# Kernel optimization log

Measured on AMD Instinct MI355X. Metric: run time of the kernel, lower is better.

## Reference

```python
import jax, jax.numpy as jnp
import numpy as np

CUTOFF = 2.0
LOG2 = float(np.log(2.0))

def ssp(x):
    # shifted softplus: softplus(x) - log(2)
    return jax.nn.softplus(x) - LOG2

def setup_inputs() -> dict:
    key = jax.random.key(0)
    ks = jax.random.split(key, 12)
    N, E, H, F, G = 10000, 320000, 256, 256, 50
    x = jax.random.normal(ks[0], (N, H), dtype=jnp.float32)
    edge_index = jax.random.randint(ks[1], (2, E), 0, N, dtype=jnp.int64)
    edge_weight = jax.random.normal(ks[2], (E, 3), dtype=jnp.float32)
    edge_attr = jax.random.normal(ks[3], (E, G), dtype=jnp.float32)
    s = lambda fan_in: 1.0 / np.sqrt(fan_in)
    mlp_w1 = jax.random.uniform(ks[4], (G, F), jnp.float32, -s(G), s(G))
    mlp_b1 = jax.random.uniform(ks[5], (F,), jnp.float32, -s(G), s(G))
    mlp_w2 = jax.random.uniform(ks[6], (F, F), jnp.float32, -s(F), s(F))
    mlp_b2 = jax.random.uniform(ks[7], (F,), jnp.float32, -s(F), s(F))
    lin1_w = jax.random.uniform(ks[8], (H, F), jnp.float32, -s(H), s(H))
    lin2_w = jax.random.uniform(ks[9], (F, H), jnp.float32, -s(F), s(F))
    lin2_b = jax.random.uniform(ks[10], (H,), jnp.float32, -s(F), s(F))
    return {"x": x, "edge_index": edge_index, "edge_weight": edge_weight,
            "edge_attr": edge_attr, "mlp_w1": mlp_w1, "mlp_b1": mlp_b1,
            "mlp_w2": mlp_w2, "mlp_b2": mlp_b2, "lin1_w": lin1_w,
            "lin2_w": lin2_w, "lin2_b": lin2_b}

def reference(x, edge_index, edge_weight, edge_attr,
              mlp_w1, mlp_b1, mlp_w2, mlp_b2, lin1_w, lin2_w, lin2_b):
    N = x.shape[0]
    # cutoff envelope on edge distances
    distances = jnp.linalg.norm(edge_weight, axis=1)                 # [E]
    C = 0.5 * (jnp.cos(distances * jnp.pi / CUTOFF) + 1.0)
    C = C * (distances <= CUTOFF)                                    # [E]
    # edge filter MLP
    W = ssp(edge_attr @ mlp_w1 + mlp_b1) @ mlp_w2 + mlp_b2           # [E, F]
    W = W * C[:, None]
    i, j = edge_index[0], edge_index[1]
    messages = W * (x[j] @ lin1_w)                                   # [E, F]
    agg = jax.ops.segment_sum(messages, i, num_segments=N)           # [N, F]
    h = ssp(agg @ lin2_w + lin2_b)                                   # [N, H]
    return x + h
```

## Files before the change

### kernel.cpp

```cpp
#include <hip/hip_runtime.h>
#include <hip/hip_bf16.h>
#include <stdint.h>

#define HF 256
#define GG 50
#define LOG2E 1.44269504088896341f
#define LN2   0.69314718055994531f

typedef __attribute__((ext_vector_type(8))) short bf16x8;
typedef __attribute__((ext_vector_type(4))) short bf16x4;
typedef __attribute__((ext_vector_type(4))) float f32x4;

__device__ __forceinline__ uint32_t f2bf2u(float a, float b){
    __hip_bfloat162 h = __float22bfloat162_rn(make_float2(a, b));
    union { __hip_bfloat162 h; uint32_t u; } v; v.h = h; return v.u;
}
__device__ __forceinline__ float bf2f(short s){
    union { uint32_t u; float f; } v; v.u = ((uint32_t)(uint16_t)s) << 16;
    return v.f;
}

__device__ __forceinline__ void pack_natural(const float* __restrict__ B,
                                             short* __restrict__ Bp,
                                             int idx, int KT, int kmax, float scale)
{
    int lane = idx & 63;
    int kt   = (idx >> 6) & (KT - 1);
    int ntg  = idx >> (6 + (KT == 2 ? 1 : 3));
    int col  = ntg * 16 + (lane & 15);
    int k0   = kt * 32 + (lane >> 4) * 8;
    uint32_t u[4];
#pragma unroll
    for (int jj = 0; jj < 4; ++jj) {
        int ka = k0 + 2*jj, kb = ka + 1;
        float a = (ka < kmax) ? B[(size_t)ka * HF + col] * scale : 0.f;
        float b = (kb < kmax) ? B[(size_t)kb * HF + col] * scale : 0.f;
        u[jj] = f2bf2u(a, b);
    }
    *(uint4*)&Bp[(size_t)idx * 8] = *(uint4*)u;
}

__global__ __launch_bounds__(256)
void prep_kernel(const float* __restrict__ w1, const float* __restrict__ b1,
                 const float* __restrict__ w2, const float* __restrict__ b2,
                 const float* __restrict__ lin1, const float* __restrict__ lin2,
                 short* __restrict__ w1p, short* __restrict__ w2p,
                 short* __restrict__ lin1p, short* __restrict__ lin2p,
                 float* __restrict__ b2p,
                 const float* __restrict__ x, short* __restrict__ x_bf, int nx8,
                 const int* __restrict__ eidx, int* __restrict__ cnt, int E,
                 float* __restrict__ agg, int nAgg4, int gConv, int gHist)
{
    int b = blockIdx.x, tid = threadIdx.x;
    if (b < 8) {
        int idx  = b * 256 + tid;
        int lane = idx & 63;
        int kt   = (idx >> 6) & 1;
        int ntg  = idx >> 7;
        int col  = ntg * 16 + (lane & 15);
        int k0   = kt * 32 + (lane >> 4) * 8;
        uint32_t u[4];
#pragma unroll
        for (int jj = 0; jj < 4; ++jj) {
            int ka = k0 + 2*jj, kb = ka + 1;
            float va = (ka < GG) ? w1[(size_t)ka * HF + col] * LOG2E
                                 : ((ka == GG) ? b1[col] * LOG2E : 0.f);
            float vb = (kb < GG) ? w1[(size_t)kb * HF + col] * LOG2E
                                 : ((kb == GG) ? b1[col] * LOG2E : 0.f);
            u[jj] = f2bf2u(va, vb);
        }
        *(uint4*)&w1p[(size_t)idx * 8] = *(uint4*)u;
    } else if (b < 40) {
        int idx = (b - 8) * 256 + tid;
        int lane = idx & 63;
        int kt   = (idx >> 6) & 7;
        int ntg  = idx >> 9;
        int col  = ntg * 16 + (lane & 15);
        int s0   = kt * 32 + (lane >> 4) * 8;
        uint32_t u[4];
#pragma unroll
        for (int jj = 0; jj < 4; ++jj) {
            int sa = s0 + 2*jj, sb = sa + 1;
            int fa = (sa >> 5) * 32 + (sa & 1) * 16 + ((sa & 31) >> 1);
            int fb = (sb >> 5) * 32 + (sb & 1) * 16 + ((sb & 31) >> 1);
            u[jj] = f2bf2u(w2[(size_t)fa * HF + col] * LN2,
                           w2[(size_t)fb * HF + col] * LN2);
        }
        *(uint4*)&w2p[(size_t)idx * 8] = *(uint4*)u;
    } else if (b < 72) {
        pack_natural(lin1, lin1p, (b - 40) * 256 + tid, 8, HF, 1.0f);
    } else if (b < 104) {
        pack_natural(lin2, lin2p, (b - 72) * 256 + tid, 8, HF, LOG2E);
    } else if (b == 104) {
        int f = tid;
        float s = 0.f;
        for (int k = 0; k < HF; ++k) {
            uint32_t r = f2bf2u(w2[(size_t)k * HF + f] * LN2, 0.f);
            s += bf2f((short)(r & 0xFFFF));
        }
        b2p[f] = b2[f] - s;
    } else if (b < 105 + gConv) {
        int idx = (b - 105) * 256 + tid;
        if (idx < nx8) {
            const float* xp = x + (size_t)idx * 8;
            float4 p0 = *(const float4*)(xp);
            float4 p1 = *(const float4*)(xp + 4);
            uint32_t u[4] = { f2bf2u(p0.x, p0.y), f2bf2u(p0.z, p0.w),
                              f2bf2u(p1.x, p1.y), f2bf2u(p1.z, p1.w) };
            *(uint4*)&x_bf[(size_t)idx * 8] = *(uint4*)u;
        }
    } else if (b < 105 + gConv + gHist) {
        int e = (b - 105 - gConv) * 256 + tid;
        if (e < E) atomicAdd(&cnt[eidx[e]], 1);
    } else {
        int idx = (b - 105 - gConv - gHist) * 256 + tid;
        if (idx < nAgg4) ((float4*)agg)[idx] = make_float4(0.f, 0.f, 0.f, 0.f);
    }
}

__global__ __launch_bounds__(256)
void scan_gemm_kernel(const int* __restrict__ cnt, int* __restrict__ row,
                      int* __restrict__ cursor, int N, int E,
                      const short* __restrict__ x_bf, const short* __restrict__ lin1p,
                      short* __restrict__ y_p)
{
    const int tid = threadIdx.x;
    if (blockIdx.x == 0) {
        __shared__ int part[256];
        const int CH = (N + 255) / 256;
        int lo = tid * CH;
        int hi = min(lo + CH, N);
        int s = 0;
        for (int n = lo; n < hi; ++n) s += cnt[n];
        part[tid] = s;
        __syncthreads();
        for (int off = 1; off < 256; off <<= 1) {
            int v = (tid >= off) ? part[tid - off] : 0;
            __syncthreads();
            part[tid] += v;
            __syncthreads();
        }
        int acc = part[tid] - s;
        for (int n = lo; n < hi; ++n) {
            row[n] = acc; cursor[n] = acc;
            acc += cnt[n];
        }
        if (tid == 255) row[N] = E;
        return;
    }
    const int blk    = blockIdx.x - 1;
    const int rowblk = blk >> 1;
    const int fh     = blk & 1;
    const int lane = tid & 63;
    const int w    = tid >> 6;
    const int l15  = lane & 15;
    const int quad = lane >> 4;
    const int row0 = rowblk * 64;

    f32x4 acc[4][2];
#pragma unroll
    for (int mt = 0; mt < 4; ++mt)
#pragma unroll
        for (int nt = 0; nt < 2; ++nt) acc[mt][nt] = (f32x4){0.f,0.f,0.f,0.f};

#pragma unroll 2
    for (int kt = 0; kt < 8; ++kt) {
        bf16x8 af[4];
#pragma unroll
        for (int mt = 0; mt < 4; ++mt) {
            int r = row0 + mt * 16 + l15;
            int rl = (r < N) ? r : 0;
            af[mt] = *(const bf16x8*)&x_bf[(size_t)rl * HF + kt * 32 + quad * 8];
        }
#pragma unroll
        for (int nt = 0; nt < 2; ++nt) {
            int ntg = fh * 8 + w * 2 + nt;
            bf16x8 bfr = *(const bf16x8*)&lin1p[(size_t)((ntg*8+kt)*64+lane)*8];
#pragma unroll
            for (int mt = 0; mt < 4; ++mt)
                acc[mt][nt] = __builtin_amdgcn_mfma_f32_16x16x32_bf16(af[mt], bfr, acc[mt][nt], 0, 0, 0);
        }
    }
    const int sbase = (fh * 2 + (w >> 1)) * 64 + l15 * 4 + (w & 1) * 2;
#pragma unroll
    for (int mt = 0; mt < 4; ++mt) {
#pragma unroll
        for (int r = 0; r < 4; ++r) {
            int row_ = row0 + mt * 16 + quad * 4 + r;
            if (row_ < N) {
                *(uint32_t*)&y_p[(size_t)row_ * HF + sbase] =
                    f2bf2u(acc[mt][0][r], acc[mt][1][r]);
            }
        }
    }
}

__global__ __launch_bounds__(256)
void scatter_kernel(const int* __restrict__ eidx, int* __restrict__ cursor,
                    int* __restrict__ perm, int E)
{
    int e = blockIdx.x * 256 + threadIdx.x;
    if (e < E) {
        int pos = atomicAdd(&cursor[eidx[e]], 1);
        perm[pos] = e;
    }
}

__global__ __launch_bounds__(256)
void node2_kernel(const float* __restrict__ agg, const short* __restrict__ lin2p,
                  const float* __restrict__ bias, const float* __restrict__ x,
                  float* __restrict__ out, int N)
{
    const int tid  = threadIdx.x;
    const int lane = tid & 63;
    const int w    = tid >> 6;
    const int l15  = lane & 15;
    const int quad = lane >> 4;
    const int row0 = ((int)blockIdx.x >> 1) * 64;
    const int fh   = blockIdx.x & 1;

    f32x4 acc[4][2];
#pragma unroll
    for (int mt = 0; mt < 4; ++mt)
#pragma unroll
        for (int nt = 0; nt < 2; ++nt) acc[mt][nt] = (f32x4){0.f,0.f,0.f,0.f};

#pragma unroll 2
    for (int kt = 0; kt < 8; ++kt) {
        bf16x8 af[4];
#pragma unroll
        for (int mt = 0; mt < 4; ++mt) {
            int r = row0 + mt * 16 + l15;
            int rl = (r < N) ? r : 0;
            const float* ap = agg + (size_t)rl * HF + kt * 32 + quad * 8;
            float4 p0 = *(const float4*)(ap);
            float4 p1 = *(const float4*)(ap + 4);
            union { uint32_t u[4]; bf16x8 v; } c;
            c.u[0] = f2bf2u(p0.x, p0.y); c.u[1] = f2bf2u(p0.z, p0.w);
            c.u[2] = f2bf2u(p1.x, p1.y); c.u[3] = f2bf2u(p1.z, p1.w);
            af[mt] = c.v;
        }
#pragma unroll
        for (int nt = 0; nt < 2; ++nt) {
            int ntg = fh * 8 + w * 2 + nt;
            bf16x8 bfr = *(const bf16x8*)&lin2p[(size_t)((ntg*8+kt)*64+lane)*8];
#pragma unroll
            for (int mt = 0; mt < 4; ++mt)
                acc[mt][nt] = __builtin_amdgcn_mfma_f32_16x16x32_bf16(af[mt], bfr, acc[mt][nt], 0, 0, 0);
        }
    }
    float bs[2];
#pragma unroll
    for (int nt = 0; nt < 2; ++nt)
        bs[nt] = LOG2E * bias[fh * 128 + w * 32 + nt * 16 + l15];
#pragma unroll
    for (int mt = 0; mt < 4; ++mt) {
#pragma unroll
        for (int r = 0; r < 4; ++r) {
            int row = row0 + mt * 16 + quad * 4 + r;
            if (row < N) {
#pragma unroll
                for (int nt = 0; nt < 2; ++nt) {
                    int f = fh * 128 + w * 32 + nt * 16 + l15;
                    float z = acc[mt][nt][r] + bs[nt];
                    float g = __builtin_amdgcn_logf(1.f + __builtin_amdgcn_exp2f(z));
                    float xv = x[(size_t)row * HF + f];
                    out[(size_t)row * HF + f] = fmaf(LN2, g, xv - LN2);
                }
            }
        }
    }
}

__global__ __launch_bounds__(512, 6)
void edge_mfma(const float* __restrict__ ea, const int* __restrict__ eidx,
               const float* __restrict__ ew,
               const short* __restrict__ w1p,
               const short* __restrict__ w2p, const float* __restrict__ b2p,
               const short* __restrict__ y_p, const int* __restrict__ perm,
               const int* __restrict__ rowp,
               float* __restrict__ agg, int E)
{
    __shared__ short smem[19584];
    short* ea_b = smem;
    short* hid  = smem;
    short* msgT = smem;
    short* St   = smem + 18432;
    __shared__ int s_e[64], s_j[64];
    __shared__ float s_c[64];
    __shared__ int s_runnode[64];
    __shared__ unsigned char s_runcomp[64];
    __shared__ unsigned long long s_bmask;
    __shared__ int s_runcnt;

    const int tid  = threadIdx.x;
    const int lane = tid & 63;
    const int w    = tid >> 6;
    const int l15  = lane & 15;
    const int quad = lane >> 4;
    const int e0   = blockIdx.x * 64;

    if (tid < 64) {
        int pp = e0 + tid;
        int e = 0, iv = -1, jv = 0;
        float c = 0.f;
        if (pp < E) {
            e  = perm[pp];
            iv = eidx[e];
            jv = eidx[E + e];
            float d0 = ew[e*3+0], d1 = ew[e*3+1], d2 = ew[e*3+2];
            float d = sqrtf(d0*d0 + d1*d1 + d2*d2);
            c = (d <= 2.0f) ? 0.5f * (__cosf(d * 1.57079632679489662f) + 1.0f) : 0.f;
        }
        s_e[tid] = e; s_j[tid] = jv; s_c[tid] = c;
        int ivn = __shfl_down(iv, 1);
        bool flag = (tid == 63) || (iv != ivn);
        unsigned long long m = __ballot(flag);
        if (flag) {
            int rid = (int)__popcll(m & ((1ull << tid) - 1ull));
            s_runnode[rid] = iv;
            int comp = 0;
            if (iv >= 0) {
                int lo = rowp[iv], hi = rowp[iv + 1];
                comp = (lo >= e0 && hi <= e0 + 64) ? 1 : 0;
            }
            s_runcomp[rid] = (unsigned char)comp;
        }
        if (tid == 0) { s_bmask = m; s_runcnt = (int)__popcll(m); }
    }
    __syncthreads();

#pragma unroll
    for (int i = 0; i < 4; ++i) {
        int idx = i * 512 + tid;
        int e = idx >> 5, q = idx & 31;
        uint32_t val;
        if (q < 25) {
            float2 v = *(const float2*)(ea + (size_t)s_e[e] * GG + q * 2);
            val = f2bf2u(v.x, v.y);
        } else {
            val = (q == 25) ? 0x00003F80u : 0u;
        }
        *(uint32_t*)&ea_b[e * 72 + q * 2] = val;
    }
    __syncthreads();

    f32x4 acc1[4][2];
#pragma unroll
    for (int mt = 0; mt < 4; ++mt)
#pragma unroll
        for (int nt = 0; nt < 2; ++nt) acc1[mt][nt] = (f32x4){0.f,0.f,0.f,0.f};

#pragma unroll
    for (int kt = 0; kt < 2; ++kt) {
        bf16x8 af[4];
#pragma unroll
        for (int mt = 0; mt < 4; ++mt)
            af[mt] = *(bf16x8*)&ea_b[(mt * 16 + l15) * 72 + kt * 32 + quad * 8];
#pragma unroll
        for (int nt = 0; nt < 2; ++nt) {
            bf16x8 bfr = *(const bf16x8*)&w1p[(size_t)(((w*2+nt)*2+kt)*64+lane)*8];
#pragma unroll
            for (int mt = 0; mt < 4; ++mt)
                acc1[mt][nt] = __builtin_amdgcn_mfma_f32_16x16x32_bf16(af[mt], bfr, acc1[mt][nt], 0, 0, 0);
        }
    }
    __syncthreads();

#pragma unroll
    for (int mt = 0; mt < 4; ++mt) {
#pragma unroll
        for (int r = 0; r < 4; ++r) {
            int e = mt * 16 + quad * 4 + r;
            float g0 = __builtin_amdgcn_logf(1.f + __builtin_amdgcn_exp2f(acc1[mt][0][r]));
            float g1 = __builtin_amdgcn_logf(1.f + __builtin_amdgcn_exp2f(acc1[mt][1][r]));
            *(uint32_t*)&hid[e * 264 + w * 32 + l15 * 2] = f2bf2u(g0, g1);
        }
    }
    __syncthreads();

    f32x4 acc2[4][2];
#pragma unroll
    for (int mt = 0; mt < 4; ++mt)
#pragma unroll
        for (int nt = 0; nt < 2; ++nt) acc2[mt][nt] = (f32x4){0.f,0.f,0.f,0.f};

    __builtin_amdgcn_s_setprio(1);
#pragma unroll 1
    for (int kt = 0; kt < 8; ++kt) {
        bf16x8 af[4];
#pragma unroll
        for (int mt = 0; mt < 4; ++mt)
            af[mt] = *(bf16x8*)&hid[(mt * 16 + l15) * 264 + kt * 32 + quad * 8];
#pragma unroll
        for (int nt = 0; nt < 2; ++nt) {
            bf16x8 bfr = *(const bf16x8*)&w2p[(size_t)(((w*2+nt)*8+kt)*64+lane)*8];
#pragma unroll
            for (int mt = 0; mt < 4; ++mt)
                acc2[mt][nt] = __builtin_amdgcn_mfma_f32_16x16x32_bf16(af[mt], bfr, acc2[mt][nt], 0, 0, 0);
        }
    }
    __builtin_amdgcn_s_setprio(0);

    uint32_t yv[4][4];
    const int ypos = (w >> 1) * 64 + l15 * 4 + (w & 1) * 2;
#pragma unroll
    for (int mt = 0; mt < 4; ++mt)
#pragma unroll
        for (int r = 0; r < 4; ++r) {
            int e = mt * 16 + quad * 4 + r;
            yv[mt][r] = *(const uint32_t*)&y_p[(size_t)s_j[e] * HF + ypos];
        }
    float bias2[2];
#pragma unroll
    for (int nt = 0; nt < 2; ++nt) bias2[nt] = b2p[w * 32 + nt * 16 + l15];

    __syncthreads();

#pragma unroll
    for (int mt = 0; mt < 4; ++mt) {
        float c0 = s_c[mt * 16 + quad * 4 + 0];
        float c1 = s_c[mt * 16 + quad * 4 + 1];
        float c2 = s_c[mt * 16 + quad * 4 + 2];
        float c3 = s_c[mt * 16 + quad * 4 + 3];
#pragma unroll
        for (int nt = 0; nt < 2; ++nt) {
            int col = w * 32 + nt * 16 + l15;
            float y0 = bf2f((short)(nt ? (yv[mt][0] >> 16) : (yv[mt][0] & 0xFFFF)));
            float y1 = bf2f((short)(nt ? (yv[mt][1] >> 16) : (yv[mt][1] & 0xFFFF)));
            float y2 = bf2f((short)(nt ? (yv[mt][2] >> 16) : (yv[mt][2] & 0xFFFF)));
            float y3 = bf2f((short)(nt ? (yv[mt][3] >> 16) : (yv[mt][3] & 0xFFFF)));
            float v0 = (acc2[mt][nt][0] + bias2[nt]) * c0 * y0;
            float v1 = (acc2[mt][nt][1] + bias2[nt]) * c1 * y1;
            float v2 = (acc2[mt][nt][2] + bias2[nt]) * c2 * y2;
            float v3 = (acc2[mt][nt][3] + bias2[nt]) * c3 * y3;
            uint2 u = make_uint2(f2bf2u(v0, v1), f2bf2u(v2, v3));
            *(uint2*)&msgT[col * 72 + mt * 16 + quad * 4] = u;
        }
    }
    {
        unsigned long long bm = s_bmask;
        int e   = tid & 63;
        int rb  = tid >> 6;
        int rid = (int)__popcll(bm & ((1ull << e) - 1ull));
#pragma unroll
        for (int q = 0; q < 2; ++q) {
            int r = rb + q * 8;
            St[r * 72 + e] = (rid == r) ? (short)0x3F80 : (short)0;
        }
    }
    __syncthreads();

    const int runcnt = s_runcnt;
    for (int ntg = 0; ntg * 16 < runcnt; ++ntg) {
        if (ntg > 0) {
            __syncthreads();
            unsigned long long bm = s_bmask;
            int e   = tid & 63;
            int rb  = tid >> 6;
            int rid = (int)__popcll(bm & ((1ull << e) - 1ull));
#pragma unroll
            for (int q = 0; q < 2; ++q) {
                int r = rb + q * 8;
                St[r * 72 + e] = (rid == ntg * 16 + r) ? (short)0x3F80 : (short)0;
            }
            __syncthreads();
        }
        f32x4 acc3[2];
#pragma unroll
        for (int mt = 0; mt < 2; ++mt) acc3[mt] = (f32x4){0.f,0.f,0.f,0.f};
#pragma unroll
        for (int kt = 0; kt < 2; ++kt) {
            bf16x8 bS = *(bf16x8*)&St[l15 * 72 + kt * 32 + quad * 8];
#pragma unroll
            for (int mt = 0; mt < 2; ++mt) {
                bf16x8 af = *(bf16x8*)&msgT[(w*32 + mt*16 + l15) * 72 + kt*32 + quad*8];
                acc3[mt] = __builtin_amdgcn_mfma_f32_16x16x32_bf16(af, bS, acc3[mt], 0, 0, 0);
            }
        }
        int r = ntg * 16 + l15;
        if (r < runcnt) {
            int node = s_runnode[r];
            if (node >= 0) {
                float* ap = agg + (size_t)node * HF + w * 32 + quad * 4;
                if (s_runcomp[r]) {
#pragma unroll
                    for (int mt = 0; mt < 2; ++mt) {
                        float4 v = make_float4(acc3[mt][0], acc3[mt][1], acc3[mt][2], acc3[mt][3]);
                        *(float4*)(ap + mt * 16) = v;
                    }
                } else {
#pragma unroll
                    for (int mt = 0; mt < 2; ++mt)
#pragma unroll
                        for (int g = 0; g < 4; ++g)
                            atomicAdd(ap + mt * 16 + g, acc3[mt][g]);
                }
            }
        }
    }
}

extern "C" void kernel_launch(void* const* d_in, const int* in_sizes, int n_in,
                              void* d_out, int out_size, void* d_ws, size_t ws_size,
                              hipStream_t stream)
{
    const float* x     = (const float*)d_in[0];
    const int*   eidx  = (const int*)  d_in[1];
    const float* ew    = (const float*)d_in[2];
    const float* ea    = (const float*)d_in[3];
    const float* w1    = (const float*)d_in[4];
    const float* b1    = (const float*)d_in[5];
    const float* w2    = (const float*)d_in[6];
    const float* b2    = (const float*)d_in[7];
    const float* lin1  = (const float*)d_in[8];
    const float* lin2  = (const float*)d_in[9];
    const float* lin2b = (const float*)d_in[10];
    float* out = (float*)d_out;

    const int N = in_sizes[0] / HF;
    const int E = in_sizes[2] / 3;

    const size_t fN = (size_t)N * HF;
    float* agg    = (float*)d_ws;
    short* y_p    = (short*)(agg + fN);
    short* x_bf   = y_p + fN;
    int*   cnt    = (int*)(x_bf + fN);
    int*   row    = cnt + N;
    int*   cursor = row + (N + 8);
    int*   perm   = cursor + N;
    short* w1p    = (short*)(((uintptr_t)(perm + E) + 255) & ~(uintptr_t)255);
    short* w2p    = w1p + 16384;
    short* lin1p  = w2p + 65536;
    short* lin2p  = lin1p + 65536;
    float* b2p    = (float*)(lin2p + 65536);

    hipMemsetAsync(cnt, 0, (size_t)N * sizeof(int), stream);

    const int nx8   = (int)(fN / 8);
    const int nAgg4 = (int)(fN / 4);
    const int gConv = (nx8 + 255) / 256;
    const int gHist = (E + 255) / 256;
    const int gZero = (nAgg4 + 255) / 256;
    prep_kernel<<<dim3(105 + gConv + gHist + gZero), dim3(256), 0, stream>>>(
        w1, b1, w2, b2, lin1, lin2, w1p, w2p, lin1p, lin2p, b2p,
        x, x_bf, nx8, eidx, cnt, E, agg, nAgg4, gConv, gHist);

    const int gNode = (N + 63) / 64;
    scan_gemm_kernel<<<dim3(1 + 2 * gNode), dim3(256), 0, stream>>>(
        cnt, row, cursor, N, E, x_bf, lin1p, y_p);

    const int gScatter = (E + 255) / 256;
    scatter_kernel<<<dim3(gScatter), dim3(256), 0, stream>>>(eidx, cursor, perm, E);

    edge_mfma<<<dim3((E + 63) / 64), dim3(512), 0, stream>>>(
        ea, eidx, ew, w1p, w2p, b2p, y_p, perm, row, agg, E);

    node2_kernel<<<dim3(2 * gNode), dim3(256), 0, stream>>>(
        agg, lin2p, lin2b, x, out, N);
}
```

Before: 325.0 us.

## Pre-sort edge attributes and metadata in scatter pass; widen node GEMM tiles

The scatter pass now computes the cutoff envelope and writes packed per-edge metadata (i, j, C) plus bf16-converted, padded edge_attr rows directly into sorted order. The edge kernel can then read contiguous rows instead of gathering through a permutation, and it drops several shared-memory staging buffers and barriers in favour of wave shuffles. The x@lin1 GEMM now runs in the same launch as the scatter, after splitting the scan into its own single-block kernel. Both node GEMMs now compute all 256 columns per block instead of splitting into halves. The cost is an extra bf16 copy of edge_attr in the workspace and an additional kernel launch.

Measured after the change: 374.8 us. 1.15x slower.

```diff
diff --git a/kernel.cpp b/kernel.cpp
--- a/kernel.cpp
+++ b/kernel.cpp
@@ -119,49 +119,84 @@
 }
 
 __global__ __launch_bounds__(256)
-void scan_gemm_kernel(const int* __restrict__ cnt, int* __restrict__ row,
-                      int* __restrict__ cursor, int N, int E,
-                      const short* __restrict__ x_bf, const short* __restrict__ lin1p,
-                      short* __restrict__ y_p)
+void scan_kernel(const int* __restrict__ cnt, int* __restrict__ row,
+                 int* __restrict__ cursor, int N, int E)
+{
+    __shared__ int part[256];
+    const int t = threadIdx.x;
+    const int CH = (N + 255) / 256;
+    int lo = t * CH;
+    int hi = min(lo + CH, N);
+    int s = 0;
+    for (int n = lo; n < hi; ++n) s += cnt[n];
+    part[t] = s;
+    __syncthreads();
+    for (int off = 1; off < 256; off <<= 1) {
+        int v = (t >= off) ? part[t - off] : 0;
+        __syncthreads();
+        part[t] += v;
+        __syncthreads();
+    }
+    int acc = part[t] - s;
+    for (int n = lo; n < hi; ++n) {
+        row[n] = acc; cursor[n] = acc;
+        acc += cnt[n];
+    }
+    if (t == 255) row[N] = E;
+}
+
+__global__ __launch_bounds__(256)
+void mid_kernel(const int* __restrict__ eidx, const float* __restrict__ ew,
+                const float* __restrict__ ea,
+                int* __restrict__ cursor, int* __restrict__ meta,
+                short* __restrict__ ea_p, int E, int gScatter,
+                const short* __restrict__ x_bf, const short* __restrict__ lin1p,
+                short* __restrict__ y_p, int N)
 {
     const int tid = threadIdx.x;
-    if (blockIdx.x == 0) {
-        __shared__ int part[256];
-        const int CH = (N + 255) / 256;
-        int lo = tid * CH;
-        int hi = min(lo + CH, N);
-        int s = 0;
-        for (int n = lo; n < hi; ++n) s += cnt[n];
-        part[tid] = s;
+    if ((int)blockIdx.x < gScatter) {
+        __shared__ int s_pos[256];
+        const int base = blockIdx.x * 256;
+        int e = base + tid;
+        int pos = 0;
+        if (e < E) {
+            int iv = eidx[e];
+            int jv = eidx[E + e];
+            float d0 = ew[e*3+0], d1 = ew[e*3+1], d2 = ew[e*3+2];
+            float d = sqrtf(d0*d0 + d1*d1 + d2*d2);
+            float c = (d <= 2.0f) ? 0.5f * (__cosf(d * 1.57079632679489662f) + 1.0f) : 0.f;
+            pos = atomicAdd(&cursor[iv], 1);
+            int4 m = make_int4(iv, jv, __float_as_int(c), 0);
+            *(int4*)&meta[(size_t)pos * 4] = m;
+        }
+        s_pos[tid] = pos;
         __syncthreads();
-        for (int off = 1; off < 256; off <<= 1) {
-            int v = (tid >= off) ? part[tid - off] : 0;
-            __syncthreads();
-            part[tid] += v;
-            __syncthreads();
-        }
-        int acc = part[tid] - s;
-        for (int n = lo; n < hi; ++n) {
-            row[n] = acc; cursor[n] = acc;
-            acc += cnt[n];
-        }
-        if (tid == 255) row[N] = E;
+        const int nloc = min(256, E - base);
+        for (int idx = tid; idx < nloc * 32; idx += 256) {
+            int el = idx >> 5, q = idx & 31;
+            uint32_t val;
+            if (q < 25) {
+                float2 v = *(const float2*)(ea + (size_t)(base + el) * GG + q * 2);
+                val = f2bf2u(v.x, v.y);
+            } else {
+                val = (q == 25) ? 0x00003F80u : 0u;
+            }
+            *(uint32_t*)&ea_p[(size_t)s_pos[el] * 64 + q * 2] = val;
+        }
         return;
     }
-    const int blk    = blockIdx.x - 1;
-    const int rowblk = blk >> 1;
-    const int fh     = blk & 1;
+    const int blk  = blockIdx.x - gScatter;
     const int lane = tid & 63;
     const int w    = tid >> 6;
     const int l15  = lane & 15;
     const int quad = lane >> 4;
-    const int row0 = rowblk * 64;
-
-    f32x4 acc[4][2];
+    const int row0 = blk * 64;
+
+    f32x4 acc[4][4];
 #pragma unroll
     for (int mt = 0; mt < 4; ++mt)
 #pragma unroll
-        for (int nt = 0; nt < 2; ++nt) acc[mt][nt] = (f32x4){0.f,0.f,0.f,0.f};
+        for (int nt = 0; nt < 4; ++nt) acc[mt][nt] = (f32x4){0.f,0.f,0.f,0.f};
 
 #pragma unroll 2
     for (int kt = 0; kt < 8; ++kt) {
@@ -173,36 +208,24 @@
             af[mt] = *(const bf16x8*)&x_bf[(size_t)rl * HF + kt * 32 + quad * 8];
         }
 #pragma unroll
-        for (int nt = 0; nt < 2; ++nt) {
-            int ntg = fh * 8 + w * 2 + nt;
-            bf16x8 bfr = *(const bf16x8*)&lin1p[(size_t)((ntg*8+kt)*64+lane)*8];
+        for (int nt = 0; nt < 4; ++nt) {
+            bf16x8 bfr = *(const bf16x8*)&lin1p[(size_t)(((w*4+nt)*8+kt)*64+lane)*8];
 #pragma unroll
             for (int mt = 0; mt < 4; ++mt)
                 acc[mt][nt] = __builtin_amdgcn_mfma_f32_16x16x32_bf16(af[mt], bfr, acc[mt][nt], 0, 0, 0);
         }
     }
-    const int sbase = (fh * 2 + (w >> 1)) * 64 + l15 * 4 + (w & 1) * 2;
 #pragma unroll
     for (int mt = 0; mt < 4; ++mt) {
 #pragma unroll
         for (int r = 0; r < 4; ++r) {
-            int row_ = row0 + mt * 16 + quad * 4 + r;
-            if (row_ < N) {
-                *(uint32_t*)&y_p[(size_t)row_ * HF + sbase] =
-                    f2bf2u(acc[mt][0][r], acc[mt][1][r]);
+            int row = row0 + mt * 16 + quad * 4 + r;
+            if (row < N) {
+                uint2 u = make_uint2(f2bf2u(acc[mt][0][r], acc[mt][1][r]),
+                                     f2bf2u(acc[mt][2][r], acc[mt][3][r]));
+                *(uint2*)&y_p[(size_t)row * HF + w * 64 + l15 * 4] = u;
             }
         }
-    }
-}
-
-__global__ __launch_bounds__(256)
-void scatter_kernel(const int* __restrict__ eidx, int* __restrict__ cursor,
-                    int* __restrict__ perm, int E)
-{
-    int e = blockIdx.x * 256 + threadIdx.x;
-    if (e < E) {
-        int pos = atomicAdd(&cursor[eidx[e]], 1);
-        perm[pos] = e;
     }
 }
 
@@ -216,14 +239,13 @@
     const int w    = tid >> 6;
     const int l15  = lane & 15;
     const int quad = lane >> 4;
-    const int row0 = ((int)blockIdx.x >> 1) * 64;
-    const int fh   = blockIdx.x & 1;
-
-    f32x4 acc[4][2];
+    const int row0 = blockIdx.x * 64;
+
+    f32x4 acc[4][4];
 #pragma unroll
     for (int mt = 0; mt < 4; ++mt)
 #pragma unroll
-        for (int nt = 0; nt < 2; ++nt) acc[mt][nt] = (f32x4){0.f,0.f,0.f,0.f};
+        for (int nt = 0; nt < 4; ++nt) acc[mt][nt] = (f32x4){0.f,0.f,0.f,0.f};
 
 #pragma unroll 2
     for (int kt = 0; kt < 8; ++kt) {
@@ -241,18 +263,16 @@
             af[mt] = c.v;
         }
 #pragma unroll
-        for (int nt = 0; nt < 2; ++nt) {
-            int ntg = fh * 8 + w * 2 + nt;
-            bf16x8 bfr = *(const bf16x8*)&lin2p[(size_t)((ntg*8+kt)*64+lane)*8];
+        for (int nt = 0; nt < 4; ++nt) {
+            bf16x8 bfr = *(const bf16x8*)&lin2p[(size_t)(((w*4+nt)*8+kt)*64+lane)*8];
 #pragma unroll
             for (int mt = 0; mt < 4; ++mt)
                 acc[mt][nt] = __builtin_amdgcn_mfma_f32_16x16x32_bf16(af[mt], bfr, acc[mt][nt], 0, 0, 0);
         }
     }
-    float bs[2];
-#pragma unroll
-    for (int nt = 0; nt < 2; ++nt)
-        bs[nt] = LOG2E * bias[fh * 128 + w * 32 + nt * 16 + l15];
+    float bs[4];
+#pragma unroll
+    for (int nt = 0; nt < 4; ++nt) bs[nt] = LOG2E * bias[w * 64 + nt * 16 + l15];
 #pragma unroll
     for (int mt = 0; mt < 4; ++mt) {
 #pragma unroll
@@ -260,8 +280,8 @@
             int row = row0 + mt * 16 + quad * 4 + r;
             if (row < N) {
 #pragma unroll
-                for (int nt = 0; nt < 2; ++nt) {
-                    int f = fh * 128 + w * 32 + nt * 16 + l15;
+                for (int nt = 0; nt < 4; ++nt) {
+                    int f = w * 64 + nt * 16 + l15;
                     float z = acc[mt][nt][r] + bs[nt];
                     float g = __builtin_amdgcn_logf(1.f + __builtin_amdgcn_exp2f(z));
                     float xv = x[(size_t)row * HF + f];
@@ -273,25 +293,19 @@
 }
 
 __global__ __launch_bounds__(512, 6)
-void edge_mfma(const float* __restrict__ ea, const int* __restrict__ eidx,
-               const float* __restrict__ ew,
+void edge_mfma(const short* __restrict__ ea_p, const int* __restrict__ meta,
                const short* __restrict__ w1p,
                const short* __restrict__ w2p, const float* __restrict__ b2p,
-               const short* __restrict__ y_p, const int* __restrict__ perm,
+               const short* __restrict__ y_p,
                const int* __restrict__ rowp,
                float* __restrict__ agg, int E)
 {
     __shared__ short smem[19584];
-    short* ea_b = smem;
     short* hid  = smem;
     short* msgT = smem;
     short* St   = smem + 18432;
-    __shared__ int s_e[64], s_j[64];
-    __shared__ float s_c[64];
     __shared__ int s_runnode[64];
     __shared__ unsigned char s_runcomp[64];
-    __shared__ unsigned long long s_bmask;
-    __shared__ int s_runcnt;
 
     const int tid  = threadIdx.x;
     const int lane = tid & 63;
@@ -300,50 +314,37 @@
     const int quad = lane >> 4;
     const int e0   = blockIdx.x * 64;
 
-    if (tid < 64) {
-        int pp = e0 + tid;
-        int e = 0, iv = -1, jv = 0;
-        float c = 0.f;
-        if (pp < E) {
-            e  = perm[pp];
-            iv = eidx[e];
-            jv = eidx[E + e];
-            float d0 = ew[e*3+0], d1 = ew[e*3+1], d2 = ew[e*3+2];
-            float d = sqrtf(d0*d0 + d1*d1 + d2*d2);
-            c = (d <= 2.0f) ? 0.5f * (__cosf(d * 1.57079632679489662f) + 1.0f) : 0.f;
-        }
-        s_e[tid] = e; s_j[tid] = jv; s_c[tid] = c;
-        int ivn = __shfl_down(iv, 1);
-        bool flag = (tid == 63) || (iv != ivn);
-        unsigned long long m = __ballot(flag);
-        if (flag) {
-            int rid = (int)__popcll(m & ((1ull << tid) - 1ull));
-            s_runnode[rid] = iv;
-            int comp = 0;
-            if (iv >= 0) {
-                int lo = rowp[iv], hi = rowp[iv + 1];
-                comp = (lo >= e0 && hi <= e0 + 64) ? 1 : 0;
-            }
-            s_runcomp[rid] = (unsigned char)comp;
-        }
-        if (tid == 0) { s_bmask = m; s_runcnt = (int)__popcll(m); }
-    }
-    __syncthreads();
-
-#pragma unroll
-    for (int i = 0; i < 4; ++i) {
-        int idx = i * 512 + tid;
-        int e = idx >> 5, q = idx & 31;
-        uint32_t val;
-        if (q < 25) {
-            float2 v = *(const float2*)(ea + (size_t)s_e[e] * GG + q * 2);
-            val = f2bf2u(v.x, v.y);
-        } else {
-            val = (q == 25) ? 0x00003F80u : 0u;
-        }
-        *(uint32_t*)&ea_b[e * 72 + q * 2] = val;
-    }
-    __syncthreads();
+    int pp = e0 + lane;
+    int4 m;
+    if (pp < E) m = *(const int4*)&meta[(size_t)pp * 4];
+    else        m = make_int4(-1, 0, 0, 0);
+    const int iv = m.x, jv = m.y;
+    const float c = __int_as_float(m.z);
+
+    int ivn = __shfl_down(iv, 1);
+    bool flag = (lane == 63) || (iv != ivn);
+    unsigned long long bm = __ballot(flag);
+    const int runcnt = (int)__popcll(bm);
+    if (w == 0 && flag) {
+        int rid = (int)__popcll(bm & ((1ull << lane) - 1ull));
+        s_runnode[rid] = iv;
+        int comp = 0;
+        if (iv >= 0) {
+            int lo = rowp[iv], hi = rowp[iv + 1];
+            comp = (lo >= e0 && hi <= e0 + 64) ? 1 : 0;
+        }
+        s_runcomp[rid] = (unsigned char)comp;
+    }
+    {
+        int e   = tid & 63;
+        int rb  = tid >> 6;
+        int rid = (int)__popcll(bm & ((1ull << e) - 1ull));
+#pragma unroll
+        for (int q = 0; q < 2; ++q) {
+            int r = rb + q * 8;
+            St[r * 72 + e] = (rid == r) ? (short)0x3F80 : (short)0;
+        }
+    }
 
     f32x4 acc1[4][2];
 #pragma unroll
@@ -355,8 +356,11 @@
     for (int kt = 0; kt < 2; ++kt) {
         bf16x8 af[4];
 #pragma unroll
-        for (int mt = 0; mt < 4; ++mt)
-            af[mt] = *(bf16x8*)&ea_b[(mt * 16 + l15) * 72 + kt * 32 + quad * 8];
+        for (int mt = 0; mt < 4; ++mt) {
+            int rowg = e0 + mt * 16 + l15;
+            if (rowg >= E) rowg = E - 1;
+            af[mt] = *(const bf16x8*)&ea_p[(size_t)rowg * 64 + kt * 32 + quad * 8];
+        }
 #pragma unroll
         for (int nt = 0; nt < 2; ++nt) {
             bf16x8 bfr = *(const bf16x8*)&w1p[(size_t)(((w*2+nt)*2+kt)*64+lane)*8];
@@ -365,7 +369,6 @@
                 acc1[mt][nt] = __builtin_amdgcn_mfma_f32_16x16x32_bf16(af[mt], bfr, acc1[mt][nt], 0, 0, 0);
         }
     }
-    __syncthreads();
 
 #pragma unroll
     for (int mt = 0; mt < 4; ++mt) {
@@ -409,7 +412,8 @@
 #pragma unroll
         for (int r = 0; r < 4; ++r) {
             int e = mt * 16 + quad * 4 + r;
-            yv[mt][r] = *(const uint32_t*)&y_p[(size_t)s_j[e] * HF + ypos];
+            int j = __shfl(jv, e);
+            yv[mt][r] = *(const uint32_t*)&y_p[(size_t)j * HF + ypos];
         }
     float bias2[2];
 #pragma unroll
@@ -419,10 +423,10 @@
 
 #pragma unroll
     for (int mt = 0; mt < 4; ++mt) {
-        float c0 = s_c[mt * 16 + quad * 4 + 0];
-        float c1 = s_c[mt * 16 + quad * 4 + 1];
-        float c2 = s_c[mt * 16 + quad * 4 + 2];
-        float c3 = s_c[mt * 16 + quad * 4 + 3];
+        float c0 = __shfl(c, mt * 16 + quad * 4 + 0);
+        float c1 = __shfl(c, mt * 16 + quad * 4 + 1);
+        float c2 = __shfl(c, mt * 16 + quad * 4 + 2);
+        float c3 = __shfl(c, mt * 16 + quad * 4 + 3);
 #pragma unroll
         for (int nt = 0; nt < 2; ++nt) {
             int col = w * 32 + nt * 16 + l15;
@@ -438,24 +442,10 @@
             *(uint2*)&msgT[col * 72 + mt * 16 + quad * 4] = u;
         }
     }
-    {
-        unsigned long long bm = s_bmask;
-        int e   = tid & 63;
-        int rb  = tid >> 6;
-        int rid = (int)__popcll(bm & ((1ull << e) - 1ull));
-#pragma unroll
-        for (int q = 0; q < 2; ++q) {
-            int r = rb + q * 8;
-            St[r * 72 + e] = (rid == r) ? (short)0x3F80 : (short)0;
-        }
-    }
-    __syncthreads();
-
-    const int runcnt = s_runcnt;
+
     for (int ntg = 0; ntg * 16 < runcnt; ++ntg) {
         if (ntg > 0) {
             __syncthreads();
-            unsigned long long bm = s_bmask;
             int e   = tid & 63;
             int rb  = tid >> 6;
             int rid = (int)__popcll(bm & ((1ull << e) - 1ull));
@@ -528,12 +518,13 @@
     int*   cnt    = (int*)(x_bf + fN);
     int*   row    = cnt + N;
     int*   cursor = row + (N + 8);
-    int*   perm   = cursor + N;
-    short* w1p    = (short*)(((uintptr_t)(perm + E) + 255) & ~(uintptr_t)255);
+    int*   meta   = (int*)(((uintptr_t)(cursor + N) + 15) & ~(uintptr_t)15);
+    short* w1p    = (short*)(((uintptr_t)(meta + 4 * (size_t)E) + 255) & ~(uintptr_t)255);
     short* w2p    = w1p + 16384;
     short* lin1p  = w2p + 65536;
     short* lin2p  = lin1p + 65536;
     float* b2p    = (float*)(lin2p + 65536);
+    short* ea_p   = (short*)(((uintptr_t)(b2p + 256) + 255) & ~(uintptr_t)255);
 
     hipMemsetAsync(cnt, 0, (size_t)N * sizeof(int), stream);
 
@@ -546,16 +537,16 @@
         w1, b1, w2, b2, lin1, lin2, w1p, w2p, lin1p, lin2p, b2p,
         x, x_bf, nx8, eidx, cnt, E, agg, nAgg4, gConv, gHist);
 
-    const int gNode = (N + 63) / 64;
-    scan_gemm_kernel<<<dim3(1 + 2 * gNode), dim3(256), 0, stream>>>(
-        cnt, row, cursor, N, E, x_bf, lin1p, y_p);
+    scan_kernel<<<dim3(1), dim3(256), 0, stream>>>(cnt, row, cursor, N, E);
 
     const int gScatter = (E + 255) / 256;
-    scatter_kernel<<<dim3(gScatter), dim3(256), 0, stream>>>(eidx, cursor, perm, E);
+    const int gNode    = (N + 63) / 64;
+    mid_kernel<<<dim3(gScatter + gNode), dim3(256), 0, stream>>>(
+        eidx, ew, ea, cursor, meta, ea_p, E, gScatter, x_bf, lin1p, y_p, N);
 
     edge_mfma<<<dim3((E + 63) / 64), dim3(512), 0, stream>>>(
-        ea, eidx, ew, w1p, w2p, b2p, y_p, perm, row, agg, E);
-
-    node2_kernel<<<dim3(2 * gNode), dim3(256), 0, stream>>>(
+        ea_p, meta, w1p, w2p, b2p, y_p, row, agg, E);
+
+    node2_kernel<<<dim3(gNode), dim3(256), 0, stream>>>(
         agg, lin2p, lin2b, x, out, N);
 }
```
